# Kernel tuning notes

Hardware: AMD Instinct MI355X
Metric: run time of the kernel (lower is better)

## Reference

```python
import jax, jax.numpy as jnp
import numpy as np

B, H, S = 2, 16, 2048
CTX = 1024
VD = 288          # valence_dim
FFN = 512         # ffn_dim
EPSILON = 0.066
LN_EPS = 1e-5


def layer_norm(x, w, b):
    mu = jnp.mean(x, axis=-1, keepdims=True)
    var = jnp.var(x, axis=-1, keepdims=True)
    return (x - mu) * jax.lax.rsqrt(var + LN_EPS) * w + b


def setup_inputs() -> dict:
    key = jax.random.key(0)
    ks = jax.random.split(key, 12)

    def lin(k, fan_in, fan_out):
        # torch nn.Linear default init: U(-1/sqrt(fan_in), 1/sqrt(fan_in)); stored as [in, out]
        bound = 1.0 / np.sqrt(fan_in)
        k1, k2 = jax.random.split(k)
        W = jax.random.uniform(k1, (fan_in, fan_out), jnp.float32, -bound, bound)
        b = jax.random.uniform(k2, (fan_out,), jnp.float32, -bound, bound)
        return W, b

    attention_scores = jax.random.normal(ks[0], (B, H, S, S), jnp.float32)
    input_ids = jax.random.randint(ks[1], (B, S), 0, CTX)

    # xavier_uniform for embedding weight [CTX, VD]
    xb = np.sqrt(6.0 / (CTX + VD))
    emb_W = jax.random.uniform(ks[2], (CTX, VD), jnp.float32, -xb, xb)

    pW1, pb1 = lin(ks[3], VD, 2 * VD)
    pW2, pb2 = lin(ks[4], 2 * VD, H)
    fW1, fb1 = lin(ks[5], H + 1, FFN)
    fW2, fb2 = lin(ks[6], FFN, FFN // 2)
    fW3, fb3 = lin(ks[7], FFN // 2, 1)

    return {
        "attention_scores": attention_scores,
        "input_ids": input_ids,
        "emb_W": emb_W,
        "ln_v_w": jnp.ones((VD,), jnp.float32),
        "ln_v_b": jnp.zeros((VD,), jnp.float32),
        "pW1": pW1, "pb1": pb1, "pW2": pW2, "pb2": pb2,
        "ln_c_w": jnp.ones((H + 1,), jnp.float32),
        "ln_c_b": jnp.zeros((H + 1,), jnp.float32),
        "fW1": fW1, "fb1": fb1, "fW2": fW2, "fb2": fb2, "fW3": fW3, "fb3": fb3,
    }


def reference(attention_scores, input_ids, emb_W, ln_v_w, ln_v_b,
              pW1, pb1, pW2, pb2, ln_c_w, ln_c_b,
              fW1, fb1, fW2, fb2, fW3, fb3):
    # token_occurrence buffer starts at zero: new_occ = 0.87*0 + clamp(counts, 1)
    counts = jnp.bincount(input_ids.reshape(-1), length=CTX).astype(jnp.float32)
    counts = jnp.maximum(counts, 1.0)
    occ = jnp.log1p(counts[input_ids])                        # [B, S]

    v = layer_norm(emb_W[input_ids], ln_v_w, ln_v_b)           # [B, S, VD]
    h = jax.nn.gelu(v @ pW1 + pb1, approximate=False)          # [B, S, 2*VD]
    valence_scores = jnp.tanh(h @ pW2 + pb2)                   # [B, S, H]

    comb = jnp.concatenate([occ[..., None], valence_scores], axis=-1)  # [B, S, H+1]
    comb = layer_norm(comb, ln_c_w, ln_c_b)

    h2 = jax.nn.gelu(comb @ fW1 + fb1, approximate=False)      # [B, S, FFN]
    h3 = jax.nn.gelu(h2 @ fW2 + fb2, approximate=False)        # [B, S, FFN//2]
    mod = jnp.tanh(h3 @ fW3 + fb3)                             # [B, S, 1]

    retrieval_weights = 1.0 + EPSILON * mod[:, None, :, :]     # [B, 1, S, 1]
    return attention_scores * retrieval_weights
```

## Files before the change

kernel.cpp:

```cpp
#include <hip/hip_runtime.h>
#include <math.h>

#define B_ 2
#define H_ 16
#define S_ 2048
#define CTX_ 1024
#define VD_ 288
#define VD2_ 576
#define FFN_ 512
#define FFNH_ 256
#define NH1_ 17
#define EPSILON_ 0.066f
#define LN_EPS_ 1e-5f
#define TPB_ 8
#define NBLK_ (B_ * S_ / TPB_)

typedef float vfloat4 __attribute__((ext_vector_type(4)));

__device__ __forceinline__ float gelu_exact(float x) {
    return 0.5f * x * (1.0f + erff(x * 0.70710678118654752440f));
}
__device__ __forceinline__ vfloat4 gelu4(vfloat4 v) {
    vfloat4 o;
    o.x = gelu_exact(v.x); o.y = gelu_exact(v.y);
    o.z = gelu_exact(v.z); o.w = gelu_exact(v.w);
    return o;
}

__global__ __launch_bounds__(1024) void count_kernel(
    const int* __restrict__ ids, int* __restrict__ counts)
{
    __shared__ int hist[CTX_];
    const int t = threadIdx.x;
    hist[t] = 0;
    __syncthreads();
    #pragma unroll
    for (int r = 0; r < (B_ * S_) / 1024; ++r)
        atomicAdd(&hist[ids[t + 1024 * r]], 1);
    __syncthreads();
    counts[t] = hist[t];
}

__global__ __launch_bounds__(512, 4) void token_mlp_kernel(
    const int* __restrict__ ids, const int* __restrict__ counts,
    const float* __restrict__ embW,
    const float* __restrict__ lnvw, const float* __restrict__ lnvb,
    const float* __restrict__ pW1, const float* __restrict__ pb1,
    const float* __restrict__ pW2, const float* __restrict__ pb2,
    const float* __restrict__ lncw, const float* __restrict__ lncb,
    const float* __restrict__ fW1, const float* __restrict__ fb1,
    const float* __restrict__ fW2, const float* __restrict__ fb2,
    const float* __restrict__ fW3, const float* __restrict__ fb3,
    float* __restrict__ wout)
{
    __shared__ __align__(16) float va[VD_][TPB_];
    __shared__ __align__(16) float ha[VD2_][TPB_];
    __shared__ __align__(16) float comb17[NH1_][TPB_];
    __shared__ __align__(16) float h2a[FFN_][TPB_];
    __shared__ __align__(16) float h3a[FFNH_][TPB_];

    const int tid  = threadIdx.x;
    const int tok0 = blockIdx.x * TPB_;
    const int wid  = tid >> 6;
    const int cthr = tid & 63;
    const int quad = wid & 1;
    const int cq   = wid >> 1;
    const int tq   = quad * 4;

    {
        const int w  = wid;
        const int l  = cthr;
        const int id = ids[tok0 + w];
        float x[5];
        float s = 0.f, sq = 0.f;
        #pragma unroll
        for (int r = 0; r < 4; ++r) {
            float xv = embW[id * VD_ + l + 64 * r];
            x[r] = xv; s += xv; sq += xv * xv;
        }
        x[4] = 0.f;
        if (l < 32) {
            float xv = embW[id * VD_ + 256 + l];
            x[4] = xv; s += xv; sq += xv * xv;
        }
        #pragma unroll
        for (int m = 32; m >= 1; m >>= 1) {
            s  += __shfl_xor(s,  m, 64);
            sq += __shfl_xor(sq, m, 64);
        }
        float mu   = s * (1.f / VD_);
        float var  = sq * (1.f / VD_) - mu * mu;
        float rstd = rsqrtf(var + LN_EPS_);
        #pragma unroll
        for (int r = 0; r < 4; ++r) {
            int i = l + 64 * r;
            va[i][w] = (x[r] - mu) * rstd * lnvw[i] + lnvb[i];
        }
        if (l < 32) {
            int i = 256 + l;
            va[i][w] = (x[4] - mu) * rstd * lnvw[i] + lnvb[i];
        }
    }
    __syncthreads();

    {
        vfloat4 a0 = 0, a1 = 0, a2 = 0;
        const int cb = 144 * cq;
        const bool extra = (cthr < 16);
        for (int k = 0; k < VD_; k += 4) {
            float w0[4], w1[4], w2[4];
            #pragma unroll
            for (int u = 0; u < 4; ++u) {
                const float* wr = &pW1[(k + u) * VD2_ + cb + cthr];
                w0[u] = wr[0]; w1[u] = wr[64];
                if (extra) w2[u] = wr[128];
            }
            vfloat4 v[4];
            #pragma unroll
            for (int u = 0; u < 4; ++u) v[u] = *(const vfloat4*)&va[k + u][tq];
            #pragma unroll
            for (int u = 0; u < 4; ++u) {
                a0 += w0[u] * v[u];
                a1 += w1[u] * v[u];
                if (extra) a2 += w2[u] * v[u];
            }
        }
        int col = cb + cthr;
        *(vfloat4*)&ha[col     ][tq] = gelu4(a0 + pb1[col]);
        *(vfloat4*)&ha[col + 64][tq] = gelu4(a1 + pb1[col + 64]);
        if (extra)
            *(vfloat4*)&ha[col + 128][tq] = gelu4(a2 + pb1[col + 128]);
    }
    __syncthreads();

    if (wid < 4) {
        const int t0  = wid * 2;
        const int col = cthr & 15;
        const int ks  = cthr >> 4;
        float2 acc = make_float2(0.f, 0.f);
        for (int k = ks * 144; k < ks * 144 + 144; k += 8) {
            float w[8]; float2 v[8];
            #pragma unroll
            for (int u = 0; u < 8; ++u) w[u] = pW2[(k + u) * H_ + col];
            #pragma unroll
            for (int u = 0; u < 8; ++u) v[u] = *(const float2*)&ha[k + u][t0];
            #pragma unroll
            for (int u = 0; u < 8; ++u) {
                acc.x += w[u] * v[u].x; acc.y += w[u] * v[u].y;
            }
        }
        acc.x += __shfl_xor(acc.x, 16, 64); acc.y += __shfl_xor(acc.y, 16, 64);
        acc.x += __shfl_xor(acc.x, 32, 64); acc.y += __shfl_xor(acc.y, 32, 64);
        if (cthr < 16) {
            float b = pb2[col];
            float2 o = make_float2(tanhf(acc.x + b), tanhf(acc.y + b));
            *(float2*)&comb17[1 + col][t0] = o;
        }
        if (cthr == 16) {
            #pragma unroll
            for (int j = 0; j < 2; ++j) {
                int t = t0 + j;
                int id = ids[tok0 + t];
                float c = (float)counts[id];
                if (c < 1.f) c = 1.f;
                comb17[0][t] = log1pf(c);
            }
        }
    }
    __syncthreads();

    if (tid < TPB_) {
        float vals[NH1_];
        float s = 0.f;
        #pragma unroll
        for (int i = 0; i < NH1_; ++i) { vals[i] = comb17[i][tid]; s += vals[i]; }
        float mu = s / NH1_;
        float vq = 0.f;
        #pragma unroll
        for (int i = 0; i < NH1_; ++i) { float d = vals[i] - mu; vq += d * d; }
        float r = rsqrtf(vq / NH1_ + LN_EPS_);
        #pragma unroll
        for (int i = 0; i < NH1_; ++i)
            comb17[i][tid] = (vals[i] - mu) * r * lncw[i] + lncb[i];
    }
    __syncthreads();

    {
        vfloat4 a0 = 0, a1 = 0;
        const int cb = 128 * cq;
        #pragma unroll
        for (int k = 0; k < NH1_; ++k) {
            vfloat4 v = *(const vfloat4*)&comb17[k][tq];
            const float* wr = &fW1[k * FFN_ + cb + cthr];
            a0 += wr[0] * v;
            a1 += wr[64] * v;
        }
        int col = cb + cthr;
        *(vfloat4*)&h2a[col     ][tq] = gelu4(a0 + fb1[col]);
        *(vfloat4*)&h2a[col + 64][tq] = gelu4(a1 + fb1[col + 64]);
    }
    __syncthreads();

    {
        vfloat4 a0 = 0;
        const int cb = 64 * cq;
        for (int k = 0; k < FFN_; k += 8) {
            float w0[8]; vfloat4 v[8];
            #pragma unroll
            for (int u = 0; u < 8; ++u)
                w0[u] = fW2[(k + u) * FFNH_ + cb + cthr];
            #pragma unroll
            for (int u = 0; u < 8; ++u) v[u] = *(const vfloat4*)&h2a[k + u][tq];
            #pragma unroll
            for (int u = 0; u < 8; ++u) a0 += w0[u] * v[u];
        }
        int col = cb + cthr;
        *(vfloat4*)&h3a[col][tq] = gelu4(a0 + fb2[col]);
    }
    __syncthreads();

    {
        const int tt = wid;
        const int l  = cthr;
        float acc = 0.f;
        #pragma unroll
        for (int r = 0; r < FFNH_ / 64; ++r) {
            int k = l + 64 * r;
            acc += h3a[k][tt] * fW3[k];
        }
        #pragma unroll
        for (int m = 32; m >= 1; m >>= 1) acc += __shfl_xor(acc, m, 64);
        if (l == 0) {
            float mod = tanhf(acc + fb3[0]);
            wout[tok0 + tt] = 1.0f + EPSILON_ * mod;
        }
    }
}

__global__ __launch_bounds__(256) void scale_kernel(
    const vfloat4* __restrict__ in, const float* __restrict__ w,
    vfloat4* __restrict__ out, long total4)
{
    long i = (long)blockIdx.x * blockDim.x + threadIdx.x;
    const long stride = (long)gridDim.x * blockDim.x;
    for (; i < total4; i += stride) {
        long row = i >> 9;
        int b = (int)(row >> 15);
        int s = (int)(row & (S_ - 1));
        float ww = w[b * S_ + s];
        vfloat4 x = __builtin_nontemporal_load(&in[i]);
        x *= ww;
        __builtin_nontemporal_store(x, &out[i]);
    }
}

extern "C" void kernel_launch(void* const* d_in, const int* in_sizes, int n_in,
                              void* d_out, int out_size, void* d_ws, size_t ws_size,
                              hipStream_t stream) {
    const float* scores = (const float*)d_in[0];
    const int*   ids    = (const int*)  d_in[1];
    const float* embW   = (const float*)d_in[2];
    const float* lnvw   = (const float*)d_in[3];
    const float* lnvb   = (const float*)d_in[4];
    const float* pW1    = (const float*)d_in[5];
    const float* pb1    = (const float*)d_in[6];
    const float* pW2    = (const float*)d_in[7];
    const float* pb2    = (const float*)d_in[8];
    const float* lncw   = (const float*)d_in[9];
    const float* lncb   = (const float*)d_in[10];
    const float* fW1    = (const float*)d_in[11];
    const float* fb1    = (const float*)d_in[12];
    const float* fW2    = (const float*)d_in[13];
    const float* fb2    = (const float*)d_in[14];
    const float* fW3    = (const float*)d_in[15];
    const float* fb3    = (const float*)d_in[16];

    int*   counts = (int*)d_ws;
    float* wout   = (float*)((char*)d_ws + CTX_ * sizeof(int));

    count_kernel<<<1, 1024, 0, stream>>>(ids, counts);
    token_mlp_kernel<<<NBLK_, 512, 0, stream>>>(
        ids, counts, embW, lnvw, lnvb, pW1, pb1, pW2, pb2,
        lncw, lncb, fW1, fb1, fW2, fb2, fW3, fb3, wout);

    long total4 = (long)B_ * H_ * S_ * S_ / 4;
    scale_kernel<<<2048, 256, 0, stream>>>(
        (const vfloat4*)scores, wout, (vfloat4*)d_out, total4);
}
```

Before: 273.9 us.

## Fuse attention-score scaling into token MLP kernel and deepen pW1 unroll

Removes the separate scale kernel. Each token-MLP block now computes its 8 retrieval weights, keeps them in shared memory, and scales the matching 8 score rows across all 16 heads itself. This drops a kernel launch and the global round trip of the weight vector, and lets the streaming traffic of one block overlap the MLP compute of other blocks. The pW1 GEMV loop is also unrolled by 8 instead of 4, which raises register pressure. In exchange, the bandwidth-bound streaming now runs inside a heavy kernel whose occupancy is limited by large shared memory and 512-thread blocks.

```diff
diff --git a/kernel.cpp b/kernel.cpp
--- a/kernel.cpp
+++ b/kernel.cpp
@@ -41,7 +41,7 @@
     counts[t] = hist[t];
 }
 
-__global__ __launch_bounds__(512, 4) void token_mlp_kernel(
+__global__ __launch_bounds__(512, 4) void token_mlp_scale_kernel(
     const int* __restrict__ ids, const int* __restrict__ counts,
     const float* __restrict__ embW,
     const float* __restrict__ lnvw, const float* __restrict__ lnvb,
@@ -51,13 +51,14 @@
     const float* __restrict__ fW1, const float* __restrict__ fb1,
     const float* __restrict__ fW2, const float* __restrict__ fb2,
     const float* __restrict__ fW3, const float* __restrict__ fb3,
-    float* __restrict__ wout)
+    const vfloat4* __restrict__ scores, vfloat4* __restrict__ out)
 {
     __shared__ __align__(16) float va[VD_][TPB_];
     __shared__ __align__(16) float ha[VD2_][TPB_];
     __shared__ __align__(16) float comb17[NH1_][TPB_];
     __shared__ __align__(16) float h2a[FFN_][TPB_];
     __shared__ __align__(16) float h3a[FFNH_][TPB_];
+    __shared__ float wl[TPB_];
 
     const int tid  = threadIdx.x;
     const int tok0 = blockIdx.x * TPB_;
@@ -107,19 +108,19 @@
         vfloat4 a0 = 0, a1 = 0, a2 = 0;
         const int cb = 144 * cq;
         const bool extra = (cthr < 16);
-        for (int k = 0; k < VD_; k += 4) {
-            float w0[4], w1[4], w2[4];
-            #pragma unroll
-            for (int u = 0; u < 4; ++u) {
+        for (int k = 0; k < VD_; k += 8) {
+            float w0[8], w1[8], w2[8];
+            #pragma unroll
+            for (int u = 0; u < 8; ++u) {
                 const float* wr = &pW1[(k + u) * VD2_ + cb + cthr];
                 w0[u] = wr[0]; w1[u] = wr[64];
                 if (extra) w2[u] = wr[128];
             }
-            vfloat4 v[4];
-            #pragma unroll
-            for (int u = 0; u < 4; ++u) v[u] = *(const vfloat4*)&va[k + u][tq];
-            #pragma unroll
-            for (int u = 0; u < 4; ++u) {
+            vfloat4 v[8];
+            #pragma unroll
+            for (int u = 0; u < 8; ++u) v[u] = *(const vfloat4*)&va[k + u][tq];
+            #pragma unroll
+            for (int u = 0; u < 8; ++u) {
                 a0 += w0[u] * v[u];
                 a1 += w1[u] * v[u];
                 if (extra) a2 += w2[u] * v[u];
@@ -230,27 +231,26 @@
         }
         #pragma unroll
         for (int m = 32; m >= 1; m >>= 1) acc += __shfl_xor(acc, m, 64);
-        if (l == 0) {
-            float mod = tanhf(acc + fb3[0]);
-            wout[tok0 + tt] = 1.0f + EPSILON_ * mod;
-        }
-    }
-}
-
-__global__ __launch_bounds__(256) void scale_kernel(
-    const vfloat4* __restrict__ in, const float* __restrict__ w,
-    vfloat4* __restrict__ out, long total4)
-{
-    long i = (long)blockIdx.x * blockDim.x + threadIdx.x;
-    const long stride = (long)gridDim.x * blockDim.x;
-    for (; i < total4; i += stride) {
-        long row = i >> 9;
-        int b = (int)(row >> 15);
-        int s = (int)(row & (S_ - 1));
-        float ww = w[b * S_ + s];
-        vfloat4 x = __builtin_nontemporal_load(&in[i]);
-        x *= ww;
-        __builtin_nontemporal_store(x, &out[i]);
+        if (l == 0)
+            wl[tt] = 1.0f + EPSILON_ * tanhf(acc + fb3[0]);
+    }
+    __syncthreads();
+
+    {
+        const int g0 = blockIdx.x * TPB_;
+        #pragma unroll 4
+        for (int m = tid; m < TPB_ * H_ * (S_ / 4); m += 512) {
+            int rr  = m >> 9;
+            int off = m & 511;
+            int j   = rr & 7;
+            int h   = rr >> 3;
+            int g   = g0 + j;
+            long row = (long)(g >> 11) * (H_ * S_) + h * S_ + (g & (S_ - 1));
+            long idx = row * (S_ / 4) + off;
+            vfloat4 x = __builtin_nontemporal_load(&scores[idx]);
+            x *= wl[j];
+            __builtin_nontemporal_store(x, &out[idx]);
+        }
     }
 }
 
@@ -275,15 +275,11 @@
     const float* fW3    = (const float*)d_in[15];
     const float* fb3    = (const float*)d_in[16];
 
-    int*   counts = (int*)d_ws;
-    float* wout   = (float*)((char*)d_ws + CTX_ * sizeof(int));
+    int* counts = (int*)d_ws;
 
     count_kernel<<<1, 1024, 0, stream>>>(ids, counts);
-    token_mlp_kernel<<<NBLK_, 512, 0, stream>>>(
+    token_mlp_scale_kernel<<<NBLK_, 512, 0, stream>>>(
         ids, counts, embW, lnvw, lnvb, pW1, pb1, pW2, pb2,
-        lncw, lncb, fW1, fb1, fW2, fb2, fW3, fb3, wout);
-
-    long total4 = (long)B_ * H_ * S_ * S_ / 4;
-    scale_kernel<<<2048, 256, 0, stream>>>(
-        (const vfloat4*)scores, wout, (vfloat4*)d_out, total4);
-}
+        lncw, lncb, fW1, fb1, fW2, fb2, fW3, fb3,
+        (const vfloat4*)scores, (vfloat4*)d_out);
+}
```

Result: faster. 249.2 us, median of 3 (-9.0%).
